# Kernel tuning notes

Measured on AMD Instinct MI355X. Metric: run time of the kernel, lower is better.

## Reference

```python
import jax, jax.numpy as jnp
import numpy as np

INPUT_DIM, HIDDEN_DIM, OUTPUT_DIM = 13, 256, 80


def setup_inputs() -> dict:
    key = jax.random.key(0)
    ks = jax.random.split(key, 5)
    x = jax.random.normal(ks[0], (64, 2048, INPUT_DIM), dtype=jnp.float32)
    # Xavier-uniform init like init_weights(); biases zero.
    def xavier(k, fan_in, fan_out):
        lim = np.sqrt(6.0 / (fan_in + fan_out)).astype(np.float32)
        return jax.random.uniform(k, (fan_in, fan_out), jnp.float32, -lim, lim)
    W1 = xavier(ks[1], INPUT_DIM, HIDDEN_DIM)
    W2 = xavier(ks[2], HIDDEN_DIM, HIDDEN_DIM)
    W3 = xavier(ks[3], HIDDEN_DIM, HIDDEN_DIM)
    W4 = xavier(ks[4], HIDDEN_DIM, OUTPUT_DIM)
    b1 = jnp.zeros((HIDDEN_DIM,), jnp.float32)
    b2 = jnp.zeros((HIDDEN_DIM,), jnp.float32)
    b3 = jnp.zeros((HIDDEN_DIM,), jnp.float32)
    b4 = jnp.zeros((OUTPUT_DIM,), jnp.float32)
    return {"x": x, "W1": W1, "b1": b1, "W2": W2, "b2": b2,
            "W3": W3, "b3": b3, "W4": W4, "b4": b4}


def reference(x, W1, b1, W2, b2, W3, b3, W4, b4):
    # Original loops over timesteps, but each timestep is an identical
    # Linear+ReLU stack -> collapse batch*seq into one batched matmul chain.
    h = jax.nn.relu(jnp.einsum('bsi,ih->bsh', x, W1) + b1)   # encoder L1
    h = jax.nn.relu(jnp.einsum('bsh,hk->bsk', h, W2) + b2)   # encoder L2
    h = jax.nn.relu(jnp.einsum('bsh,hk->bsk', h, W3) + b3)   # decoder L1
    out = jnp.einsum('bsh,ho->bso', h, W4) + b4              # decoder L2 (no ReLU)
    return out
```

## Files before the change

kernel.cpp:

```cpp
#include <hip/hip_runtime.h>


typedef _Float16 half_t;
typedef _Float16 half8 __attribute__((ext_vector_type(8)));
typedef float f32x16 __attribute__((ext_vector_type(16)));
typedef unsigned int uint4v __attribute__((ext_vector_type(4)));

#define M_TOTAL (64*2048)

__global__ void prep_w(const float* __restrict__ W1, const float* __restrict__ W2,
                       const float* __restrict__ W3, const float* __restrict__ W4,
                       half_t* __restrict__ wp) {
    int tid = blockIdx.x * 256 + threadIdx.x;
    if (tid >= 312 * 512) return;
    int blk = tid >> 9, r = tid & 511;
    int lane = r >> 3, j = r & 7;
    const float* W; int K, N, nt, ks;
    if (blk < 8)        { W = W1; K = 13;  N = 256; nt = blk;              ks = 0; }
    else if (blk < 136) { W = W2; K = 256; N = 256; nt = (blk-8) >> 4;     ks = (blk-8) & 15; }
    else if (blk < 264) { W = W3; K = 256; N = 256; nt = (blk-136) >> 4;   ks = (blk-136) & 15; }
    else                { W = W4; K = 256; N = 80;  nt = (blk-264) >> 4;   ks = (blk-264) & 15; }
    int k = ks * 16 + (lane >> 5) * 8 + j;
    int n = nt * 32 + (lane & 31);
    float v = (k < K && n < N) ? W[k * N + n] : 0.f;
    wp[tid] = (half_t)v;
}


__device__ __forceinline__ unsigned int pkrtz(float a, float b) {
    auto p = __builtin_amdgcn_cvt_pkrtz(a, b);
    return __builtin_bit_cast(unsigned int, p);
}

typedef const __attribute__((address_space(1))) unsigned int guint_t;
typedef __attribute__((address_space(3))) unsigned int luint_t;

__device__ __forceinline__ void stage_strip(const half_t* __restrict__ g,
                                            half_t* l, int bytes, int tid) {
    const char* gc = (const char*)g;
    char* lc = (char*)l;
    const int go = tid * 16;
    const int lo = (tid >> 6) << 10;
#pragma unroll
    for (int r = 0; r < bytes; r += 4096) {
        __builtin_amdgcn_global_load_lds((guint_t*)(gc + r + go),
                                         (luint_t*)(lc + r + lo), 16, 0, 0);
    }
}

__device__ __forceinline__ int strip_off(int s) {
    if (s == 0)  return 0;
    if (s <= 8)  return (8   + (s - 1)  * 16) * 512;
    if (s <= 16) return (136 + (s - 9)  * 16) * 512;
    return (264 + (s - 17) * 16) * 512;
}

template <int NKS, bool RELU>
__device__ __forceinline__ void dense_tile(const half_t* astrip,
                                           const unsigned int (&Bin)[16][4],
                                           unsigned int (*Bout)[4],
                                           const float* biasnt, int lane, bool hi)
{
    f32x16 acc = {};
#pragma unroll
    for (int ks = 0; ks < NKS; ++ks) {
        half8 a = *(const half8*)(astrip + ((ks * 64 + lane) << 3));
        uint4v bw = { Bin[ks][0], Bin[ks][1], Bin[ks][2], Bin[ks][3] };
        acc = __builtin_amdgcn_mfma_f32_32x32x16_f16(a, __builtin_bit_cast(half8, bw),
                                                     acc, 0, 0, 0);
    }
#pragma unroll
    for (int s = 0; s < 2; ++s) {
        float v[8];
#pragma unroll
        for (int q = 0; q < 8; ++q) {
            int f = (q & 3) + 8 * (q >> 2) + (hi ? 4 : 0);
            float t = acc[8 * s + q] + biasnt[16 * s + f];
            v[q] = RELU ? fmaxf(t, 0.f) : t;
        }
        unsigned int P0 = pkrtz(v[0], v[1]);
        unsigned int P1 = pkrtz(v[2], v[3]);
        unsigned int P2 = pkrtz(v[4], v[5]);
        unsigned int P3 = pkrtz(v[6], v[7]);
        unsigned int t0 = __shfl_xor(P0, 32);
        unsigned int t1 = __shfl_xor(P1, 32);
        unsigned int t2 = __shfl_xor(P2, 32);
        unsigned int t3 = __shfl_xor(P3, 32);
        Bout[s][0] = hi ? t2 : P0;
        Bout[s][1] = hi ? t3 : P1;
        Bout[s][2] = hi ? P2 : t0;
        Bout[s][3] = hi ? P3 : t1;
    }
}

__global__ __launch_bounds__(256, 2) void mlp_mfma(
    const float* __restrict__ x, const half_t* __restrict__ wp,
    const float* __restrict__ b1, const float* __restrict__ b2,
    const float* __restrict__ b3, const float* __restrict__ b4,
    float* __restrict__ out)
{
    __shared__ half_t wbuf[2][8192];
    __shared__ float  bias_lds[864];
    __shared__ float  obuf[4][32 * 33];

    const int tid  = threadIdx.x;
    const int lane = tid & 63;
    const int wave = tid >> 6;
    const bool hi  = lane >= 32;
    const int m0   = (blockIdx.x * 4 + wave) * 32;

    bias_lds[tid] = b1[tid];
    bias_lds[256 + tid] = b2[tid];
    bias_lds[512 + tid] = b3[tid];
    if (tid < 96) bias_lds[768 + tid] = (tid < 80) ? b4[tid] : 0.f;

    stage_strip(wp + strip_off(0), wbuf[0], 8192, tid);

    unsigned int BA[16][4], BB[16][4];

    {
        const float* xp = x + (long)(m0 + (lane & 31)) * 13;
        float xv[8];
        if (!hi) {
#pragma unroll
            for (int j = 0; j < 8; ++j) xv[j] = xp[j];
        } else {
#pragma unroll
            for (int j = 0; j < 5; ++j) xv[j] = xp[8 + j];
            xv[5] = xv[6] = xv[7] = 0.f;
        }
        BA[0][0] = pkrtz(xv[0], xv[1]);
        BA[0][1] = pkrtz(xv[2], xv[3]);
        BA[0][2] = pkrtz(xv[4], xv[5]);
        BA[0][3] = pkrtz(xv[6], xv[7]);
    }

    __syncthreads();

    stage_strip(wp + strip_off(1), wbuf[1], 16384, tid);
#pragma unroll
    for (int nt = 0; nt < 8; ++nt)
        dense_tile<1, true>(&wbuf[0][nt * 512], BA, &BB[2 * nt],
                            bias_lds + nt * 32, lane, hi);
    __syncthreads();

#pragma unroll
    for (int nt = 0; nt < 8; ++nt) {
        stage_strip(wp + strip_off(2 + nt), wbuf[(2 + nt) & 1], 16384, tid);
        dense_tile<16, true>(&wbuf[(1 + nt) & 1][0], BB, &BA[2 * nt],
                             bias_lds + 256 + nt * 32, lane, hi);
        __syncthreads();
    }

#pragma unroll
    for (int nt = 0; nt < 8; ++nt) {
        stage_strip(wp + strip_off(10 + nt), wbuf[(10 + nt) & 1], 16384, tid);
        dense_tile<16, true>(&wbuf[(9 + nt) & 1][0], BA, &BB[2 * nt],
                             bias_lds + 512 + nt * 32, lane, hi);
        __syncthreads();
    }

#pragma unroll
    for (int nt = 0; nt < 3; ++nt) {
        if (nt < 2) stage_strip(wp + strip_off(18 + nt), wbuf[(18 + nt) & 1], 16384, tid);
        const half_t* astrip = &wbuf[(17 + nt) & 1][0];
        f32x16 acc = {};
#pragma unroll
        for (int ks = 0; ks < 16; ++ks) {
            half8 a = *(const half8*)(astrip + ((ks * 64 + lane) << 3));
            uint4v bw = { BB[ks][0], BB[ks][1], BB[ks][2], BB[ks][3] };
            acc = __builtin_amdgcn_mfma_f32_32x32x16_f16(a, __builtin_bit_cast(half8, bw),
                                                         acc, 0, 0, 0);
        }
#pragma unroll
        for (int reg = 0; reg < 16; ++reg) {
            int rr = (reg & 3) + 8 * (reg >> 2) + (hi ? 4 : 0);
            obuf[wave][(lane & 31) * 33 + rr] = acc[reg] + bias_lds[768 + nt * 32 + rr];
        }
        __syncthreads();
#pragma unroll
        for (int i = 0; i < 16; ++i) {
            int idx = i * 64 + lane;
            int m = idx >> 5, c = idx & 31;
            int f = nt * 32 + c;
            if (f < 80)
                out[(long)(m0 + m) * 80 + f] = obuf[wave][m * 33 + c];
        }
        __syncthreads();
    }
}


extern "C" void kernel_launch(void* const* d_in, const int* in_sizes, int n_in,
                              void* d_out, int out_size, void* d_ws, size_t ws_size,
                              hipStream_t stream) {
    const float* x  = (const float*)d_in[0];
    const float* W1 = (const float*)d_in[1];
    const float* b1 = (const float*)d_in[2];
    const float* W2 = (const float*)d_in[3];
    const float* b2 = (const float*)d_in[4];
    const float* W3 = (const float*)d_in[5];
    const float* b3 = (const float*)d_in[6];
    const float* W4 = (const float*)d_in[7];
    const float* b4 = (const float*)d_in[8];
    float* out = (float*)d_out;

    half_t* wp = (half_t*)d_ws;

    hipLaunchKernelGGL(prep_w, dim3(624), dim3(256), 0, stream, W1, W2, W3, W4, wp);
    hipLaunchKernelGGL(mlp_mfma, dim3(M_TOTAL / 128), dim3(256), 0, stream,
                       x, wp, b1, b2, b3, b4, out);
}
```

Baseline: 60.85 us.

## Triple-buffer weight strips with vmcnt-based barriers and direct output stores

Weight staging moves from two LDS buffers to three, so each strip is prefetched two stages ahead. Full __syncthreads are replaced by partial s_waitcnt vmcnt plus s_barrier, which lets the next strip's loads stay in flight. The cross-half lane exchange now uses permlane32_swap instead of four shuffles. The output layer writes results straight to global memory from registers rather than through an LDS transpose buffer with extra barriers. This trades more LDS use and uncoalesced output stores for fewer barriers and more load overlap.

```diff
diff --git a/kernel.cpp b/kernel.cpp
--- a/kernel.cpp
+++ b/kernel.cpp
@@ -5,6 +5,7 @@
 typedef _Float16 half8 __attribute__((ext_vector_type(8)));
 typedef float f32x16 __attribute__((ext_vector_type(16)));
 typedef unsigned int uint4v __attribute__((ext_vector_type(4)));
+typedef int int2v __attribute__((ext_vector_type(2)));
 
 #define M_TOTAL (64*2048)
 
@@ -55,6 +56,13 @@
     return (264 + (s - 17) * 16) * 512;
 }
 
+#define PIPE_BAR(Nstr) do {                                   \
+    asm volatile("s_waitcnt vmcnt(" Nstr ")" ::: "memory");   \
+    __builtin_amdgcn_sched_barrier(0);                        \
+    __builtin_amdgcn_s_barrier();                             \
+    __builtin_amdgcn_sched_barrier(0);                        \
+} while (0)
+
 template <int NKS, bool RELU>
 __device__ __forceinline__ void dense_tile(const half_t* astrip,
                                            const unsigned int (&Bin)[16][4],
@@ -82,14 +90,34 @@
         unsigned int P1 = pkrtz(v[2], v[3]);
         unsigned int P2 = pkrtz(v[4], v[5]);
         unsigned int P3 = pkrtz(v[6], v[7]);
-        unsigned int t0 = __shfl_xor(P0, 32);
-        unsigned int t1 = __shfl_xor(P1, 32);
-        unsigned int t2 = __shfl_xor(P2, 32);
-        unsigned int t3 = __shfl_xor(P3, 32);
-        Bout[s][0] = hi ? t2 : P0;
-        Bout[s][1] = hi ? t3 : P1;
-        Bout[s][2] = hi ? P2 : t0;
-        Bout[s][3] = hi ? P3 : t1;
+        int2v r02 = __builtin_amdgcn_permlane32_swap((int)P0, (int)P2, false, false);
+        int2v r13 = __builtin_amdgcn_permlane32_swap((int)P1, (int)P3, false, false);
+        Bout[s][0] = (unsigned int)r02.x;
+        Bout[s][1] = (unsigned int)r13.x;
+        Bout[s][2] = (unsigned int)r02.y;
+        Bout[s][3] = (unsigned int)r13.y;
+    }
+}
+
+__device__ __forceinline__ void out_tile(const half_t* astrip,
+                                         const unsigned int (&Bin)[16][4],
+                                         const float* biasnt, float* __restrict__ out,
+                                         int m0, int nt, int lane, bool hi)
+{
+    f32x16 acc = {};
+#pragma unroll
+    for (int ks = 0; ks < 16; ++ks) {
+        half8 a = *(const half8*)(astrip + ((ks * 64 + lane) << 3));
+        uint4v bw = { Bin[ks][0], Bin[ks][1], Bin[ks][2], Bin[ks][3] };
+        acc = __builtin_amdgcn_mfma_f32_32x32x16_f16(a, __builtin_bit_cast(half8, bw),
+                                                     acc, 0, 0, 0);
+    }
+    float* orow = out + (long)(m0 + (lane & 31)) * 80 + nt * 32;
+#pragma unroll
+    for (int reg = 0; reg < 16; ++reg) {
+        if (nt == 2 && (reg >> 2) >= 2) continue;
+        int rr = (reg & 3) + 8 * (reg >> 2) + (hi ? 4 : 0);
+        orow[rr] = acc[reg] + biasnt[rr];
     }
 }
 
@@ -99,15 +127,13 @@
     const float* __restrict__ b3, const float* __restrict__ b4,
     float* __restrict__ out)
 {
-    __shared__ half_t wbuf[2][8192];
+    __shared__ half_t wbuf[3][8192];
     __shared__ float  bias_lds[864];
-    __shared__ float  obuf[4][32 * 33];
 
     const int tid  = threadIdx.x;
     const int lane = tid & 63;
-    const int wave = tid >> 6;
     const bool hi  = lane >= 32;
-    const int m0   = (blockIdx.x * 4 + wave) * 32;
+    const int m0   = (blockIdx.x * 4 + (tid >> 6)) * 32;
 
     bias_lds[tid] = b1[tid];
     bias_lds[256 + tid] = b2[tid];
@@ -115,6 +141,7 @@
     if (tid < 96) bias_lds[768 + tid] = (tid < 80) ? b4[tid] : 0.f;
 
     stage_strip(wp + strip_off(0), wbuf[0], 8192, tid);
+    stage_strip(wp + strip_off(1), wbuf[1], 16384, tid);
 
     unsigned int BA[16][4], BB[16][4];
 
@@ -137,56 +164,37 @@
 
     __syncthreads();
 
-    stage_strip(wp + strip_off(1), wbuf[1], 16384, tid);
+    stage_strip(wp + strip_off(2), wbuf[2], 16384, tid);
 #pragma unroll
     for (int nt = 0; nt < 8; ++nt)
         dense_tile<1, true>(&wbuf[0][nt * 512], BA, &BB[2 * nt],
                             bias_lds + nt * 32, lane, hi);
-    __syncthreads();
-
-#pragma unroll
-    for (int nt = 0; nt < 8; ++nt) {
-        stage_strip(wp + strip_off(2 + nt), wbuf[(2 + nt) & 1], 16384, tid);
-        dense_tile<16, true>(&wbuf[(1 + nt) & 1][0], BB, &BA[2 * nt],
-                             bias_lds + 256 + nt * 32, lane, hi);
-        __syncthreads();
-    }
-
-#pragma unroll
-    for (int nt = 0; nt < 8; ++nt) {
-        stage_strip(wp + strip_off(10 + nt), wbuf[(10 + nt) & 1], 16384, tid);
-        dense_tile<16, true>(&wbuf[(9 + nt) & 1][0], BA, &BB[2 * nt],
-                             bias_lds + 512 + nt * 32, lane, hi);
-        __syncthreads();
-    }
-
-#pragma unroll
-    for (int nt = 0; nt < 3; ++nt) {
-        if (nt < 2) stage_strip(wp + strip_off(18 + nt), wbuf[(18 + nt) & 1], 16384, tid);
-        const half_t* astrip = &wbuf[(17 + nt) & 1][0];
-        f32x16 acc = {};
-#pragma unroll
-        for (int ks = 0; ks < 16; ++ks) {
-            half8 a = *(const half8*)(astrip + ((ks * 64 + lane) << 3));
-            uint4v bw = { BB[ks][0], BB[ks][1], BB[ks][2], BB[ks][3] };
-            acc = __builtin_amdgcn_mfma_f32_32x32x16_f16(a, __builtin_bit_cast(half8, bw),
-                                                         acc, 0, 0, 0);
-        }
-#pragma unroll
-        for (int reg = 0; reg < 16; ++reg) {
-            int rr = (reg & 3) + 8 * (reg >> 2) + (hi ? 4 : 0);
-            obuf[wave][(lane & 31) * 33 + rr] = acc[reg] + bias_lds[768 + nt * 32 + rr];
-        }
-        __syncthreads();
-#pragma unroll
-        for (int i = 0; i < 16; ++i) {
-            int idx = i * 64 + lane;
-            int m = idx >> 5, c = idx & 31;
-            int f = nt * 32 + c;
-            if (f < 80)
-                out[(long)(m0 + m) * 80 + f] = obuf[wave][m * 33 + c];
-        }
-        __syncthreads();
+
+#pragma unroll
+    for (int i = 0; i < 8; ++i) {
+        const int k = 1 + i;
+        PIPE_BAR("4");
+        stage_strip(wp + strip_off(k + 2), wbuf[(k + 2) % 3], 16384, tid);
+        dense_tile<16, true>(&wbuf[k % 3][0], BB, &BA[2 * i],
+                             bias_lds + 256 + i * 32, lane, hi);
+    }
+
+#pragma unroll
+    for (int i = 0; i < 8; ++i) {
+        const int k = 9 + i;
+        PIPE_BAR("4");
+        stage_strip(wp + strip_off(k + 2), wbuf[(k + 2) % 3], 16384, tid);
+        dense_tile<16, true>(&wbuf[k % 3][0], BA, &BB[2 * i],
+                             bias_lds + 512 + i * 32, lane, hi);
+    }
+
+#pragma unroll
+    for (int i = 0; i < 3; ++i) {
+        const int k = 17 + i;
+        if (i < 2) PIPE_BAR("4");
+        else       PIPE_BAR("0");
+        if (i == 0) stage_strip(wp + strip_off(19), wbuf[19 % 3], 16384, tid);
+        out_tile(&wbuf[k % 3][0], BB, bias_lds + 768 + i * 32, out, m0, i, lane, hi);
     }
 }
 
```

After: 53.73 us. 1.13x faster.
